# Kernel tuning notes

Hardware: AMD Instinct MI355X
Metric: run time of the kernel (lower is better)

The kernel has to match this reference:

```python
import jax, jax.numpy as jnp
import numpy as np
from jax import lax


def setup_inputs() -> dict:
    key = jax.random.key(0)
    kw, ku, kk, kv = jax.random.split(key, 4)
    B, H, W, C = 8, 16, 16, 256
    # w is a positive per-channel decay (offset keeps exp(sum relu(...)) numerically sane);
    # k, u scaled down like trained RWKV params to avoid exp overflow in the reference.
    w = jax.random.uniform(kw, (C,), dtype=jnp.float32) + 0.3
    u = jax.random.normal(ku, (C,), dtype=jnp.float32) * 0.1
    k = jax.random.normal(kk, (B, H, W, C), dtype=jnp.float32) * 0.1
    v = jax.random.normal(kv, (B, H, W, C), dtype=jnp.float32)
    return {"B": B, "H": H, "W": W, "C": C, "w": w, "u": u, "k": k, "v": v}


def _wkv2d(B, H, W, C, w, u, k, v):
    # kernel covers the whole feature map
    K = 2 * (max(H, W) - 1) + 1
    pad = K // 2
    c = K // 2
    # Manhattan-distance decay weights, (C, K, K), with bonus u at the center.
    coords = jnp.arange(K)
    dist = (jnp.abs(coords[None, :] - c) + jnp.abs(coords[:, None] - c)).astype(w.dtype)
    wmat = -dist[None, :, :] * w[:, None, None]
    wmat = wmat.at[:, c, c].add(u)
    wflat = wmat.reshape(C, K * K).T  # (K*K, C)

    k_chw = jnp.transpose(k, (0, 3, 1, 2))  # (B,C,H,W)
    k_pad = jnp.pad(k_chw, ((0, 0), (0, 0), (pad, pad), (pad, pad)))  # zero pad == F.unfold padding

    idx = jnp.arange(K * K, dtype=jnp.int32)
    dys, dxs = idx // K, idx % K

    # Fused windowed relu-sum: never materialize the (B,C,K^2,HW) unfold tensor.
    def body(acc, xs):
        dy, dx, wc = xs
        win = lax.dynamic_slice(k_pad, (0, 0, dy, dx), (B, C, H, W))
        return acc + jax.nn.relu(win + wc[None, :, None, None]), None

    acc0 = jnp.zeros((B, C, H, W), dtype=k.dtype)
    k_adj, _ = lax.scan(body, acc0, (dys, dxs, wflat))

    v_chw = jnp.transpose(v, (0, 3, 1, 2))
    out = jnp.exp(k_adj) * v_chw  # (B,C,H,W)
    return jnp.transpose(out, (0, 2, 3, 1))  # back to (B,H,W,C)


def reference(B, H, W, C, w, u, k, v):
    return _wkv2d(B, H, W, C, w, u, k, v)
```

## Files before the change

### kernel.cpp

```cpp
#include <hip/hip_runtime.h>
#include <math.h>


constexpr int Bq = 8, Hq = 16, Wq = 16, Cq = 256;
constexpr int HW = Hq * Wq;
constexpr int CT = 4;

__global__ __launch_bounds__(256, 2)
void wkv2d_kernel(const float* __restrict__ w,
                  const float* __restrict__ u,
                  const float* __restrict__ k,
                  const float* __restrict__ v,
                  float* __restrict__ out) {
    __shared__ float klds[HW * CT];

    const int bid = blockIdx.x;
    const int cg  = bid & 63;
    const int b   = bid >> 6;
    const int c0  = cg * CT;

    const int tid  = threadIdx.x;
    const int wave = tid >> 6;
    const int lane = tid & 63;
    const int x    = lane & 15;
    const int y0   = (lane >> 4) << 2;

    {
        const float4* src = (const float4*)(k + (size_t)b * HW * Cq + c0);
        ((float4*)klds)[tid] = src[(size_t)tid * (Cq / 4)];
    }
    __syncthreads();

    const int c   = c0 + wave;
    const float wc = w[c];
    const float uc = u[c];

    float wx[16];
    #pragma unroll
    for (int rx = 0; rx < 16; ++rx)
        wx[rx] = fabsf((float)(rx - x)) * wc;

    float yif[4];
    #pragma unroll
    for (int i = 0; i < 4; ++i) yif[i] = (float)(y0 + i);

    float acc[4] = {0.f, 0.f, 0.f, 0.f};

    for (int ry = 0; ry < 16; ++ry) {
        const float fy = (float)ry;
        float wy[4];
        #pragma unroll
        for (int i = 0; i < 4; ++i)
            wy[i] = fabsf(fy - yif[i]) * wc;

        #pragma unroll
        for (int rx = 0; rx < 16; ++rx) {
            const float kk = klds[(ry * 16 + rx) * CT + wave];
            const float t0 = kk - wx[rx];
            #pragma unroll
            for (int i = 0; i < 4; ++i)
                acc[i] += fmaxf(t0 - wy[i], 0.f);
        }
    }

    #pragma unroll
    for (int i = 0; i < 4; ++i) {
        const float ks = klds[((y0 + i) * 16 + x) * CT + wave];
        acc[i] += fmaxf(ks + uc, 0.f) - fmaxf(ks, 0.f);
    }

    #pragma unroll
    for (int i = 0; i < 4; ++i) {
        const size_t idx = ((size_t)((b * 16 + (y0 + i)) * 16 + x)) * Cq + c;
        out[idx] = __expf(acc[i]) * v[idx];
    }
}

extern "C" void kernel_launch(void* const* d_in, const int* in_sizes, int n_in,
                              void* d_out, int out_size, void* d_ws, size_t ws_size,
                              hipStream_t stream) {
    const float* w = (const float*)d_in[4];
    const float* u = (const float*)d_in[5];
    const float* k = (const float*)d_in[6];
    const float* v = (const float*)d_in[7];
    float* out = (float*)d_out;

    const int grid = Bq * (Cq / CT);
    wkv2d_kernel<<<grid, 256, 0, stream>>>(w, u, k, v, out);
}
```

Baseline: 86.51 us.

## Split source rows across wave pairs with LDS reduction and vectorized row loads

Each block now handles 2 channels instead of 4. Two waves per channel each sum over half of the 16 source rows, and their partial sums are combined through shared memory before the epilogue. The grid doubles to 1024 blocks, launch bounds target higher occupancy, and LDS is laid out per channel so a whole source row can be read with float4 loads instead of scalar reads. The cost is an extra barrier and LDS round trip, and half the waves sit idle during the epilogue.

```diff
diff --git a/kernel.cpp b/kernel.cpp
--- a/kernel.cpp
+++ b/kernel.cpp
@@ -4,75 +4,91 @@
 
 constexpr int Bq = 8, Hq = 16, Wq = 16, Cq = 256;
 constexpr int HW = Hq * Wq;
-constexpr int CT = 4;
+constexpr int CT = 2;
 
-__global__ __launch_bounds__(256, 2)
+__global__ __launch_bounds__(256, 4)
 void wkv2d_kernel(const float* __restrict__ w,
                   const float* __restrict__ u,
                   const float* __restrict__ k,
                   const float* __restrict__ v,
                   float* __restrict__ out) {
-    __shared__ float klds[HW * CT];
+    __shared__ float  klds[CT][HW];
+    __shared__ float4 pacc[CT][64];
 
     const int bid = blockIdx.x;
-    const int cg  = bid & 63;
-    const int b   = bid >> 6;
+    const int cg  = bid & 127;
+    const int b   = bid >> 7;
     const int c0  = cg * CT;
 
     const int tid  = threadIdx.x;
-    const int wave = tid >> 6;
+    const int wid  = tid >> 6;
     const int lane = tid & 63;
+    const int cc   = wid & 1;
+    const int h    = wid >> 1;
     const int x    = lane & 15;
     const int y0   = (lane >> 4) << 2;
 
     {
-        const float4* src = (const float4*)(k + (size_t)b * HW * Cq + c0);
-        ((float4*)klds)[tid] = src[(size_t)tid * (Cq / 4)];
+        const float2 kv = *(const float2*)(k + ((size_t)(b * HW + tid)) * Cq + c0);
+        klds[0][tid] = kv.x;
+        klds[1][tid] = kv.y;
     }
     __syncthreads();
 
-    const int c   = c0 + wave;
+    const int   c  = c0 + cc;
     const float wc = w[c];
-    const float uc = u[c];
 
     float wx[16];
     #pragma unroll
     for (int rx = 0; rx < 16; ++rx)
         wx[rx] = fabsf((float)(rx - x)) * wc;
 
-    float yif[4];
+    float acc[4] = {0.f, 0.f, 0.f, 0.f};
+    const int ry0 = h * 8;
+
     #pragma unroll
-    for (int i = 0; i < 4; ++i) yif[i] = (float)(y0 + i);
-
-    float acc[4] = {0.f, 0.f, 0.f, 0.f};
-
-    for (int ry = 0; ry < 16; ++ry) {
+    for (int rr = 0; rr < 8; ++rr) {
+        const int   ry = ry0 + rr;
         const float fy = (float)ry;
         float wy[4];
         #pragma unroll
         for (int i = 0; i < 4; ++i)
-            wy[i] = fabsf(fy - yif[i]) * wc;
+            wy[i] = fabsf(fy - (float)(y0 + i)) * wc;
+
+        float4 row[4];
+        #pragma unroll
+        for (int j = 0; j < 4; ++j)
+            row[j] = ((const float4*)&klds[cc][ry * 16])[j];
 
         #pragma unroll
-        for (int rx = 0; rx < 16; ++rx) {
-            const float kk = klds[(ry * 16 + rx) * CT + wave];
-            const float t0 = kk - wx[rx];
+        for (int j = 0; j < 4; ++j) {
+            const float rv[4] = {row[j].x, row[j].y, row[j].z, row[j].w};
             #pragma unroll
-            for (int i = 0; i < 4; ++i)
-                acc[i] += fmaxf(t0 - wy[i], 0.f);
+            for (int t = 0; t < 4; ++t) {
+                const float t0 = rv[t] - wx[j * 4 + t];
+                #pragma unroll
+                for (int i = 0; i < 4; ++i)
+                    acc[i] += fmaxf(t0 - wy[i], 0.f);
+            }
         }
     }
 
-    #pragma unroll
-    for (int i = 0; i < 4; ++i) {
-        const float ks = klds[((y0 + i) * 16 + x) * CT + wave];
-        acc[i] += fmaxf(ks + uc, 0.f) - fmaxf(ks, 0.f);
+    if (h == 1) {
+        pacc[cc][lane] = make_float4(acc[0], acc[1], acc[2], acc[3]);
     }
+    __syncthreads();
 
-    #pragma unroll
-    for (int i = 0; i < 4; ++i) {
-        const size_t idx = ((size_t)((b * 16 + (y0 + i)) * 16 + x)) * Cq + c;
-        out[idx] = __expf(acc[i]) * v[idx];
+    if (h == 0) {
+        const float4 p  = pacc[cc][lane];
+        const float  uc = u[c];
+        float tot[4] = {acc[0] + p.x, acc[1] + p.y, acc[2] + p.z, acc[3] + p.w};
+        #pragma unroll
+        for (int i = 0; i < 4; ++i) {
+            const float ks = klds[cc][(y0 + i) * 16 + x];
+            float a = tot[i] + fmaxf(ks + uc, 0.f) - fmaxf(ks, 0.f);
+            const size_t idx = ((size_t)((b * 16 + (y0 + i)) * 16 + x)) * Cq + c;
+            out[idx] = __expf(a) * v[idx];
+        }
     }
 }
 
```

After: 86.09 us. About the same (-0.5%).

## Split work over output row pairs and 16-channel groups with transposed LDS

Applied to the files above, without the earlier changes.

Replaces the grid of 512 blocks (4 channels each, one wave per channel, 4 output rows per thread) with 1024 blocks covering 16 channels and 2 output rows. The k slice is transposed into LDS as per-channel padded rows so each thread reads float4 vectors of its own channel. Occupancy hint is raised to 4 blocks per CU. The aim is more parallelism across the GPU and cheaper LDS reads. The cost is that each block reloads the whole k tile for only 2 rows, and each thread does less work per load.

```diff
diff --git a/kernel.cpp b/kernel.cpp
--- a/kernel.cpp
+++ b/kernel.cpp
@@ -4,76 +4,85 @@
 
 constexpr int Bq = 8, Hq = 16, Wq = 16, Cq = 256;
 constexpr int HW = Hq * Wq;
-constexpr int CT = 4;
+constexpr int CG = 16;
+constexpr int YT = 2;
+constexpr int ROWP = HW + 4;
 
-__global__ __launch_bounds__(256, 2)
+__global__ __launch_bounds__(256, 4)
 void wkv2d_kernel(const float* __restrict__ w,
                   const float* __restrict__ u,
                   const float* __restrict__ k,
                   const float* __restrict__ v,
                   float* __restrict__ out) {
-    __shared__ float klds[HW * CT];
+    __shared__ float klds[CG][ROWP];
 
     const int bid = blockIdx.x;
-    const int cg  = bid & 63;
-    const int b   = bid >> 6;
-    const int c0  = cg * CT;
+    const int y0  = (bid & 7) * YT;
+    const int c0  = ((bid >> 3) & 15) * CG;
+    const int b   = bid >> 7;
 
-    const int tid  = threadIdx.x;
-    const int wave = tid >> 6;
-    const int lane = tid & 63;
-    const int x    = lane & 15;
-    const int y0   = (lane >> 4) << 2;
+    const int tid = threadIdx.x;
+    const int cl  = tid & 15;
+    const int x   = tid >> 4;
 
     {
-        const float4* src = (const float4*)(k + (size_t)b * HW * Cq + c0);
-        ((float4*)klds)[tid] = src[(size_t)tid * (Cq / 4)];
+        #pragma unroll
+        for (int i = 0; i < 4; ++i) {
+            const int f = tid + 256 * i;
+            const int p = f >> 2;
+            const int q = f & 3;
+            const float4 kv = ((const float4*)(k + ((size_t)(b * HW + p)) * Cq + c0))[q];
+            klds[4 * q + 0][p] = kv.x;
+            klds[4 * q + 1][p] = kv.y;
+            klds[4 * q + 2][p] = kv.z;
+            klds[4 * q + 3][p] = kv.w;
+        }
     }
     __syncthreads();
 
-    const int c   = c0 + wave;
+    const int   c  = c0 + cl;
     const float wc = w[c];
-    const float uc = u[c];
+    const float fx = (float)x;
+    const float fy0 = (float)y0;
 
-    float wx[16];
+    float wxv[16];
     #pragma unroll
     for (int rx = 0; rx < 16; ++rx)
-        wx[rx] = fabsf((float)(rx - x)) * wc;
+        wxv[rx] = fabsf((float)rx - fx) * wc;
 
-    float yif[4];
+    float acc0 = 0.f, acc1 = 0.f;
+    const float* krow = &klds[cl][0];
+
     #pragma unroll
-    for (int i = 0; i < 4; ++i) yif[i] = (float)(y0 + i);
+    for (int ry = 0; ry < 16; ++ry) {
+        const float fy  = (float)ry;
+        const float wy0 = fabsf(fy - fy0) * wc;
+        const float wy1 = fabsf(fy - fy0 - 1.0f) * wc;
 
-    float acc[4] = {0.f, 0.f, 0.f, 0.f};
-
-    for (int ry = 0; ry < 16; ++ry) {
-        const float fy = (float)ry;
-        float wy[4];
+        const float4* rr = (const float4*)(krow + ry * 16);
         #pragma unroll
-        for (int i = 0; i < 4; ++i)
-            wy[i] = fabsf(fy - yif[i]) * wc;
-
-        #pragma unroll
-        for (int rx = 0; rx < 16; ++rx) {
-            const float kk = klds[(ry * 16 + rx) * CT + wave];
-            const float t0 = kk - wx[rx];
+        for (int j = 0; j < 4; ++j) {
+            const float4 r = rr[j];
+            const float rv[4] = {r.x, r.y, r.z, r.w};
             #pragma unroll
-            for (int i = 0; i < 4; ++i)
-                acc[i] += fmaxf(t0 - wy[i], 0.f);
+            for (int t = 0; t < 4; ++t) {
+                const float t0 = rv[t] - wxv[4 * j + t];
+                acc0 += fmaxf(t0 - wy0, 0.f);
+                acc1 += fmaxf(t0 - wy1, 0.f);
+            }
         }
     }
 
-    #pragma unroll
-    for (int i = 0; i < 4; ++i) {
-        const float ks = klds[((y0 + i) * 16 + x) * CT + wave];
-        acc[i] += fmaxf(ks + uc, 0.f) - fmaxf(ks, 0.f);
-    }
+    const float uc  = u[c];
+    const float ks0 = krow[(y0 + 0) * 16 + x];
+    const float ks1 = krow[(y0 + 1) * 16 + x];
+    const float a0 = acc0 + fmaxf(ks0 + uc, 0.f) - fmaxf(ks0, 0.f);
+    const float a1 = acc1 + fmaxf(ks1 + uc, 0.f) - fmaxf(ks1, 0.f);
 
-    #pragma unroll
-    for (int i = 0; i < 4; ++i) {
-        const size_t idx = ((size_t)((b * 16 + (y0 + i)) * 16 + x)) * Cq + c;
-        out[idx] = __expf(acc[i]) * v[idx];
-    }
+    const size_t idx0 = ((size_t)((b * 16 + y0) * 16 + x)) * Cq + c;
+    const size_t idx1 = idx0 + (size_t)Wq * Cq;
+    out[idx0] = __expf(a0) * v[idx0];
+    out[idx1] = __expf(a1) * v[idx1];
 }
 
 extern "C" void kernel_launch(void* const* d_in, const int* in_sizes, int n_in,
@@ -85,6 +94,6 @@
     const float* v = (const float*)d_in[7];
     float* out = (float*)d_out;
 
-    const int grid = Bq * (Cq / CT);
+    const int grid = Bq * (Cq / CG) * (Hq / YT);
     wkv2d_kernel<<<grid, 256, 0, stream>>>(w, u, k, v, out);
 }
```

New measurement: 81.09 us. -6.3%, faster.
